# Optimization experiments

Hardware: AMD Instinct MI355X
Metric: run time of the kernel (lower is better)

Reference implementation:

```python
import jax, jax.numpy as jnp
import numpy as np

HEADS, DIM_HEADS = 16, 16
SCALE = DIM_HEADS ** -0.5

# (forward_perm, inverse_perm) for each axial dim of x: (B, S, E, H, W)
# axial axes are 1 (seq), 3 (H=4), 4 (W=5); emb axis 2 moved to last, axial axis to second-last
_PERMS = [
    ((0, 3, 4, 1, 2), (0, 3, 4, 1, 2)),  # seq axis (self-inverse)
    ((0, 1, 4, 3, 2), (0, 1, 4, 3, 2)),  # H axis (self-inverse)
    ((0, 1, 3, 4, 2), (0, 1, 4, 2, 3)),  # W axis
]


def _self_attn(x, wq, wkv, wo_w, wo_b):
    # x: (..., t, d); standard multi-head self-attention along t
    q = x @ wq.T                               # (..., t, 256)
    k, v = jnp.split(x @ wkv.T, 2, axis=-1)    # each (..., t, 256)
    lead, tlen = x.shape[:-2], x.shape[-2]
    sh = (*lead, tlen, HEADS, DIM_HEADS)
    q, k, v = q.reshape(sh), k.reshape(sh), v.reshape(sh)
    scores = jnp.einsum('...thd,...shd->...hts', q, k) * SCALE
    attn = jax.nn.softmax(scores, axis=-1)
    o = jnp.einsum('...hts,...shd->...thd', attn, v)
    o = o.reshape(*lead, tlen, HEADS * DIM_HEADS)
    return o @ wo_w.T + wo_b


def _axial_attention_layer(x, wq_l, wkv_l, wo_w_l, wo_b_l):
    # sum of attention along each axial dim (sum_axial_out=True)
    out = jnp.zeros_like(x)
    for a, (p, ip) in enumerate(_PERMS):
        y = jnp.transpose(x, p)
        y = _self_attn(y, wq_l[a], wkv_l[a], wo_w_l[a], wo_b_l[a])
        out = out + jnp.transpose(y, ip)
    return out


def setup_inputs() -> dict:
    key = jax.random.key(0)
    ks = jax.random.split(key, 8)
    B, S, E, H, W = 32, 64, 256, 4, 5
    return {
        'x': jax.random.normal(ks[0], (B, S, E, H, W), jnp.float32),
        'pos_s': jax.random.normal(ks[1], (1, S, E, 1, 1), jnp.float32),
        'pos_h': jax.random.normal(ks[2], (1, 1, E, H, 1), jnp.float32),
        'pos_w': jax.random.normal(ks[3], (1, 1, E, 1, W), jnp.float32),
        'wq': jax.random.normal(ks[4], (2, 3, 256, E), jnp.float32) * 0.02,
        'wkv': jax.random.normal(ks[5], (2, 3, 512, E), jnp.float32) * 0.02,
        'wo_w': jax.random.normal(ks[6], (2, 3, E, 256), jnp.float32) * 0.02,
        'wo_b': jnp.zeros((2, 3, E), jnp.float32),
        'dec_w': jax.random.normal(ks[7], (1, E), jnp.float32) * 0.02,
        'dec_b': jnp.zeros((1,), jnp.float32),
    }


def reference(x, pos_s, pos_h, pos_w, wq, wkv, wo_w, wo_b, dec_w, dec_b):
    # additive axial positional embeddings
    x = x + pos_s + pos_h + pos_w
    # two stacked AxialAttention blocks (no residual in the wrapper)
    for l in range(2):
        x = _axial_attention_layer(x, wq[l], wkv[l], wo_w[l], wo_b[l])
    # (B, S, E, H, W) -> (B, S, H, W, E), linear decode to 1 channel, sigmoid
    x = jnp.transpose(x, (0, 1, 3, 4, 2))
    return jax.nn.sigmoid(x @ dec_w.T + dec_b)
```

## Files before the change

kernel.cpp:

```cpp
#include <hip/hip_runtime.h>
#include <stdint.h>

typedef unsigned short u16;
typedef u16 u16x8 __attribute__((ext_vector_type(8)));
typedef __bf16 bf16x8 __attribute__((ext_vector_type(8)));
typedef float f32x4 __attribute__((ext_vector_type(4)));
typedef float f32x16 __attribute__((ext_vector_type(16)));

#define NE   256
#define NPOS 40960

__device__ __forceinline__ float bf2f(u16 h) {
  union { unsigned u; float f; } c; c.u = ((unsigned)h) << 16; return c.f;
}
__device__ __forceinline__ u16 f2bf(float f) {
  union { float f; unsigned u; } c; c.f = f;
  unsigned u = c.u;
  return (u16)((u + 0x7FFFu + ((u >> 16) & 1u)) >> 16);
}
__device__ __forceinline__ unsigned pkbf(float a, float b) {
  unsigned r;
  asm("v_cvt_pk_bf16_f32 %0, %1, %2" : "=v"(r) : "v"(a), "v"(b));
  return r;
}
__device__ __forceinline__ void gll16(const void* g, void* l) {
  __builtin_amdgcn_global_load_lds(
      (const __attribute__((address_space(1))) void*)g,
      (__attribute__((address_space(3))) void*)l, 16, 0, 0);
}

__global__ __launch_bounds__(256) void prep_kernel(
    const float* __restrict__ x, const float* __restrict__ pos_s,
    const float* __restrict__ pos_h, const float* __restrict__ pos_w,
    u16* __restrict__ xb)
{
  __shared__ float Ls[256 * 21];
  const int bs = blockIdx.x;
  const int s  = bs & 63;
  const int tid = threadIdx.x;
  const float* xp = x + (size_t)bs * 5120;
  for (int i = tid; i < 5120; i += 256) {
    int e = i / 20, hw = i % 20;
    int h = hw / 5, w = hw % 5;
    float v = xp[i] + pos_s[s * 256 + e] + pos_h[e * 4 + h] + pos_w[e * 5 + w];
    Ls[e * 21 + hw] = v;
  }
  __syncthreads();
  u16* op = xb + (size_t)bs * 20 * 256;
  for (int i = tid; i < 5120; i += 256) {
    int nl = i >> 8, e = i & 255;
    op[nl * 256 + e] = f2bf(Ls[e * 21 + nl]);
  }
}

__global__ __launch_bounds__(256) void pack_qkv(
    const float* __restrict__ wq, const float* __restrict__ wkv, u16* __restrict__ dst)
{
  int i = blockIdx.x * 256 + threadIdx.x;
  int la = i / (768 * 256);
  int rem = i - la * (768 * 256);
  int r = rem >> 8, c = rem & 255;
  float v = (r < 256) ? wq[(size_t)la * 65536 + r * 256 + c]
                      : wkv[(size_t)la * 131072 + (r - 256) * 256 + c];
  dst[i] = f2bf(v);
}

__global__ __launch_bounds__(256) void pack_wo(
    const float* __restrict__ wo, u16* __restrict__ dst)
{
  int i = blockIdx.x * 256 + threadIdx.x;
  int l = i / 196608;
  int rem = i - l * 196608;
  int out = rem / 768, k = rem % 768;
  int a = k >> 8, in = k & 255;
  dst[i] = f2bf(wo[(size_t)(((l * 3 + a) * 256) + out) * 256 + in]);
}

__global__ __launch_bounds__(256) void pack_bias(
    const float* __restrict__ wo_b, float* __restrict__ bsum)
{
  int i = blockIdx.x * 256 + threadIdx.x;
  if (i < 512) {
    int l = i >> 8, c = i & 255;
    bsum[i] = wo_b[(l * 3 + 0) * 256 + c] + wo_b[(l * 3 + 1) * 256 + c]
            + wo_b[(l * 3 + 2) * 256 + c];
  }
}

template<int MODE>
__global__ __launch_bounds__(256, 2) void gemm_bt(
    const u16* __restrict__ A, const u16* __restrict__ B,
    u16* __restrict__ Cb, float* __restrict__ Cf,
    const float* __restrict__ bias, int K, int ldc)
{
  __shared__ alignas(16) u16 As[128 * 32];
  __shared__ alignas(16) u16 Bs[128 * 32];
  const int tid  = threadIdx.x;
  const int bm   = blockIdx.x, bn = blockIdx.y;
  const int lane = tid & 63, w = tid >> 6;
  const int wr   = (w >> 1) * 64, wc = (w & 1) * 64;
  const int r16  = lane & 15, khi = lane >> 4;

  f32x4 acc[4][4] = {};

  const u16* gA = A + (size_t)bm * 128 * K;
  const u16* gB = B + (size_t)bn * 128 * K;

  const int nkt = K >> 5;
  for (int kt = 0; kt < nkt; ++kt) {
    const u16* tA = gA + kt * 32;
    const u16* tB = gB + kt * 32;
    for (int i = tid; i < 512; i += 256) {
      int row = i >> 2, seg = (i & 3) << 3;
      gll16(tA + (size_t)row * K + seg, (char*)As + i * 16);
      gll16(tB + (size_t)row * K + seg, (char*)Bs + i * 16);
    }
    asm volatile("s_waitcnt vmcnt(0)" ::: "memory");
    __syncthreads();

    bf16x8 af[4], bfr[4];
    #pragma unroll
    for (int m = 0; m < 4; ++m)
      af[m] = *(const bf16x8*)(As + (wr + m * 16 + r16) * 32 + khi * 8);
    #pragma unroll
    for (int n = 0; n < 4; ++n)
      bfr[n] = *(const bf16x8*)(Bs + (wc + n * 16 + r16) * 32 + khi * 8);
    #pragma unroll
    for (int m = 0; m < 4; ++m)
      #pragma unroll
      for (int n = 0; n < 4; ++n)
        acc[m][n] = __builtin_amdgcn_mfma_f32_16x16x32_bf16(af[m], bfr[n], acc[m][n], 0, 0, 0);
    __syncthreads();
  }

  const int row0 = bm * 128 + wr + khi * 4;
  const int col0 = bn * 128 + wc + r16;
  #pragma unroll
  for (int m = 0; m < 4; ++m) {
    #pragma unroll
    for (int n = 0; n < 4; ++n) {
      int c = col0 + n * 16;
      float bv = (MODE != 0) ? bias[c] : 0.f;
      #pragma unroll
      for (int j = 0; j < 4; ++j) {
        int r = row0 + m * 16 + j;
        if (MODE == 0)      Cb[(size_t)r * ldc + c] = f2bf(acc[m][n][j]);
        else if (MODE == 1) Cf[(size_t)r * ldc + c] = acc[m][n][j] + bv;
        else                Cb[(size_t)r * ldc + c] = f2bf(acc[m][n][j] + bv);
      }
    }
  }
}

__global__ __launch_bounds__(256) void attn_seq_mfma(
    const u16* __restrict__ QKV, u16* __restrict__ Ob)
{
  const int w = threadIdx.x >> 6, lane = threadIdx.x & 63;
  const int wid = blockIdx.x * 4 + w;
  const int hd = wid & 15, g = wid >> 4;
  const int gb = g / 20, gr = g % 20;
  const int nbase = gb * 1280 + gr;
  const int lo = lane & 31, hi = lane >> 5;

  bf16x8 kf[2], qf[2];
  #pragma unroll
  for (int t = 0; t < 2; ++t) {
    size_t r = (size_t)(nbase + (lo + 32 * t) * 20) * 768;
    kf[t] = *(const bf16x8*)(QKV + r + 256 + hd * 16 + hi * 8);
    qf[t] = *(const bf16x8*)(QKV + r +       hd * 16 + hi * 8);
  }
  union { u16 a[8]; bf16x8 v; } vt[4];
  #pragma unroll
  for (int c = 0; c < 4; ++c)
    #pragma unroll
    for (int j = 0; j < 8; ++j)
      vt[c].a[j] = QKV[(size_t)(nbase + (c * 16 + hi * 8 + j) * 20) * 768
                       + 512 + hd * 16 + lo];

  f32x16 s00 = {}, s10 = {}, s01 = {}, s11 = {};
  s00 = __builtin_amdgcn_mfma_f32_32x32x16_bf16(kf[0], qf[0], s00, 0, 0, 0);
  s10 = __builtin_amdgcn_mfma_f32_32x32x16_bf16(kf[1], qf[0], s10, 0, 0, 0);
  s01 = __builtin_amdgcn_mfma_f32_32x32x16_bf16(kf[0], qf[1], s01, 0, 0, 0);
  s11 = __builtin_amdgcn_mfma_f32_32x32x16_bf16(kf[1], qf[1], s11, 0, 0, 0);

  auto run_qt = [&](f32x16 t0, f32x16 t1, int qt) {
    float m = -1e30f;
    #pragma unroll
    for (int r = 0; r < 16; ++r) { m = fmaxf(m, t0[r]); m = fmaxf(m, t1[r]); }
    m = fmaxf(m, __shfl_xor(m, 32));
    const float C = 0.36067376022f;
    float mc = m * C;
    float sum = 0.f;
    #pragma unroll
    for (int r = 0; r < 16; ++r) {
      float p0 = __builtin_amdgcn_exp2f(t0[r] * C - mc);
      float p1 = __builtin_amdgcn_exp2f(t1[r] * C - mc);
      t0[r] = p0; t1[r] = p1; sum += p0; sum += p1;
    }
    sum += __shfl_xor(sum, 32);
    float inv = __builtin_amdgcn_rcpf(sum);
    #pragma unroll
    for (int r = 0; r < 16; ++r) { t0[r] *= inv; t1[r] *= inv; }

    f32x16 oa = {};
    #pragma unroll
    for (int c = 0; c < 4; ++c) {
      const int rb = 8 * (c & 1);
      const f32x16& tt = (c < 2) ? t0 : t1;
      unsigned X0 = pkbf(tt[rb + 0], tt[rb + 1]);
      unsigned X1 = pkbf(tt[rb + 2], tt[rb + 3]);
      unsigned Y0 = pkbf(tt[rb + 4], tt[rb + 5]);
      unsigned Y1 = pkbf(tt[rb + 6], tt[rb + 7]);
      unsigned X0p = __shfl_xor((int)X0, 32), X1p = __shfl_xor((int)X1, 32);
      unsigned Y0p = __shfl_xor((int)Y0, 32), Y1p = __shfl_xor((int)Y1, 32);
      union { unsigned u[4]; bf16x8 v; } pf;
      pf.u[0] = hi ? Y0p : X0;
      pf.u[1] = hi ? Y1p : X1;
      pf.u[2] = hi ? Y0  : X0p;
      pf.u[3] = hi ? Y1  : X1p;
      oa = __builtin_amdgcn_mfma_f32_32x32x16_bf16(vt[c].v, pf.v, oa, 0, 0, 0);
    }
    unsigned P0 = pkbf(oa[0], oa[1]);
    unsigned P1 = pkbf(oa[2], oa[3]);
    unsigned P2 = pkbf(oa[4], oa[5]);
    unsigned P3 = pkbf(oa[6], oa[7]);
    unsigned sP0 = __shfl_xor((int)P0, 32), sP1 = __shfl_xor((int)P1, 32);
    unsigned sP2 = __shfl_xor((int)P2, 32), sP3 = __shfl_xor((int)P3, 32);
    union { unsigned u[4]; u16x8 v; } ov;
    ov.u[0] = hi ? sP2 : P0;
    ov.u[1] = hi ? sP3 : P1;
    ov.u[2] = hi ? P2  : sP0;
    ov.u[3] = hi ? P3  : sP1;
    u16* po = Ob + (size_t)(nbase + (qt * 32 + lo) * 20) * 768 + hd * 16 + hi * 8;
    *(u16x8*)po = ov.v;
  };
  run_qt(s00, s10, 0);
  run_qt(s01, s11, 1);
}

template<int AXIS, int T>
__global__ __launch_bounds__(256) void attn_small(
    const u16* __restrict__ QKV, u16* __restrict__ O)
{
  const int tg = blockIdx.x * 256 + threadIdx.x;
  const int hd = tg & 15, n = tg >> 4;
  int base, stp;
  if (AXIS == 1) { int h = (n % 20) / 5; base = n - h * 5; stp = 5; }
  else           { int w5 = n % 5;       base = n - w5;    stp = 1; }

  const u16* qp = QKV + (size_t)n * 768 + hd * 16;
  u16x8 q0 = *(const u16x8*)(qp), q1 = *(const u16x8*)(qp + 8);
  float q[16];
  #pragma unroll
  for (int d = 0; d < 8; ++d) { q[d] = bf2f(q0[d]) * 0.25f; q[d + 8] = bf2f(q1[d]) * 0.25f; }

  float s[T];
  float m = -1e30f;
  #pragma unroll
  for (int j = 0; j < T; ++j) {
    const u16* kp = QKV + (size_t)(base + j * stp) * 768 + 256 + hd * 16;
    u16x8 k0 = *(const u16x8*)(kp), k1 = *(const u16x8*)(kp + 8);
    float a = 0.f;
    #pragma unroll
    for (int d = 0; d < 8; ++d) a += q[d] * bf2f(k0[d]) + q[d + 8] * bf2f(k1[d]);
    s[j] = a;
    m = fmaxf(m, a);
  }
  float sum = 0.f;
  float o[16];
  #pragma unroll
  for (int d = 0; d < 16; ++d) o[d] = 0.f;
  #pragma unroll
  for (int j = 0; j < T; ++j) {
    float pj = __expf(s[j] - m);
    sum += pj;
    const u16* vp = QKV + (size_t)(base + j * stp) * 768 + 512 + hd * 16;
    u16x8 w0 = *(const u16x8*)(vp), w1 = *(const u16x8*)(vp + 8);
    #pragma unroll
    for (int d = 0; d < 8; ++d) { o[d] += pj * bf2f(w0[d]); o[d + 8] += pj * bf2f(w1[d]); }
  }
  float inv = 1.0f / sum;
  u16x8 r0, r1;
  #pragma unroll
  for (int d = 0; d < 8; ++d) { r0[d] = f2bf(o[d] * inv); r1[d] = f2bf(o[d + 8] * inv); }
  u16* po = O + (size_t)n * 768 + hd * 16;
  *(u16x8*)(po)     = r0;
  *(u16x8*)(po + 8) = r1;
}

__global__ __launch_bounds__(256) void decode_kernel(
    const float* __restrict__ xt, const float* __restrict__ dec_w,
    const float* __restrict__ dec_b, float* __restrict__ out)
{
  int wid  = threadIdx.x >> 6;
  int lane = threadIdx.x & 63;
  int n = blockIdx.x * 4 + wid;
  float4 a = *(const float4*)(xt + (size_t)n * NE + lane * 4);
  float4 b = *(const float4*)(dec_w + lane * 4);
  float acc = a.x * b.x + a.y * b.y + a.z * b.z + a.w * b.w;
  #pragma unroll
  for (int m = 1; m < 64; m <<= 1) acc += __shfl_xor(acc, m);
  if (lane == 0) out[n] = 1.0f / (1.0f + __expf(-(acc + dec_b[0])));
}

extern "C" void kernel_launch(void* const* d_in, const int* in_sizes, int n_in,
                              void* d_out, int out_size, void* d_ws, size_t ws_size,
                              hipStream_t stream) {
  const float* x     = (const float*)d_in[0];
  const float* pos_s = (const float*)d_in[1];
  const float* pos_h = (const float*)d_in[2];
  const float* pos_w = (const float*)d_in[3];
  const float* wq    = (const float*)d_in[4];
  const float* wkv   = (const float*)d_in[5];
  const float* wo_w  = (const float*)d_in[6];
  const float* wo_b  = (const float*)d_in[7];
  const float* dec_w = (const float*)d_in[8];
  const float* dec_b = (const float*)d_in[9];
  float* out = (float*)d_out;

  char* ws = (char*)d_ws;
  u16*   xb   = (u16*)ws;
  u16*   Ob   = (u16*)(ws + 20971520);
  u16*   QKV  = (u16*)(ws + 83886080);
  u16*   wqp  = (u16*)(ws + 146800768);
  u16*   wop  = (u16*)(ws + 149160064);
  float* bsum = (float*)(ws + 149946496);
  float* acc  = (float*)(ws + 83886080);

  prep_kernel<<<2048, 256, 0, stream>>>(x, pos_s, pos_h, pos_w, xb);
  pack_qkv<<<4608, 256, 0, stream>>>(wq, wkv, wqp);
  pack_wo<<<1536, 256, 0, stream>>>(wo_w, wop);
  pack_bias<<<2, 256, 0, stream>>>(wo_b, bsum);

  for (int l = 0; l < 2; ++l) {
    for (int a = 0; a < 3; ++a) {
      int la = l * 3 + a;
      gemm_bt<0><<<dim3(320, 6), 256, 0, stream>>>(
          xb, wqp + (size_t)la * 196608, QKV, nullptr, nullptr, 256, 768);
      if (a == 0)      attn_seq_mfma<<<2560, 256, 0, stream>>>(QKV, Ob);
      else if (a == 1) attn_small<1, 4><<<2560, 256, 0, stream>>>(QKV, Ob + 256);
      else             attn_small<2, 5><<<2560, 256, 0, stream>>>(QKV, Ob + 512);
    }
    if (l == 0)
      gemm_bt<3><<<dim3(320, 2), 256, 0, stream>>>(
          Ob, wop, xb, nullptr, bsum, 768, 256);
    else
      gemm_bt<1><<<dim3(320, 2), 256, 0, stream>>>(
          Ob, wop + 196608, nullptr, acc, bsum + 256, 768, 256);
  }

  decode_kernel<<<NPOS / 4, 256, 0, stream>>>(acc, dec_w, dec_b, out);
}
```

Measured before the change: 385.4 us.

## Batch H/W axis QKV projections, fuse decode into output GEMM epilogue

Merges the H- and W-axis QKV projections into one wider GEMM (1536-wide QKV row) and one combined attention kernel, cutting launches and reducing small-grid tail effects. Folds the 1/sqrt(d) query scale into the packed wq weights. Replaces the final fp32 output write plus separate decode pass with a per-tile dot against dec_w and atomic adds into a logit buffer, followed by a tiny sigmoid kernel. This removes the fp32 activation round-trip, but adds atomics and a memset and doubles the QKV workspace.

```diff
diff --git a/kernel.cpp b/kernel.cpp
--- a/kernel.cpp
+++ b/kernel.cpp
@@ -9,6 +9,7 @@
 
 #define NE   256
 #define NPOS 40960
+#define QLD  1536
 
 __device__ __forceinline__ float bf2f(u16 h) {
   union { unsigned u; float f; } c; c.u = ((unsigned)h) << 16; return c.f;
@@ -60,7 +61,7 @@
   int la = i / (768 * 256);
   int rem = i - la * (768 * 256);
   int r = rem >> 8, c = rem & 255;
-  float v = (r < 256) ? wq[(size_t)la * 65536 + r * 256 + c]
+  float v = (r < 256) ? wq[(size_t)la * 65536 + r * 256 + c] * 0.25f
                       : wkv[(size_t)la * 131072 + (r - 256) * 256 + c];
   dst[i] = f2bf(v);
 }
@@ -90,8 +91,9 @@
 template<int MODE>
 __global__ __launch_bounds__(256, 2) void gemm_bt(
     const u16* __restrict__ A, const u16* __restrict__ B,
-    u16* __restrict__ Cb, float* __restrict__ Cf,
-    const float* __restrict__ bias, int K, int ldc)
+    u16* __restrict__ Cb, const float* __restrict__ bias,
+    const float* __restrict__ dw, float* __restrict__ logit,
+    int K, int ldc)
 {
   __shared__ alignas(16) u16 As[128 * 32];
   __shared__ alignas(16) u16 Bs[128 * 32];
@@ -135,18 +137,41 @@
 
   const int row0 = bm * 128 + wr + khi * 4;
   const int col0 = bn * 128 + wc + r16;
-  #pragma unroll
-  for (int m = 0; m < 4; ++m) {
+
+  if constexpr (MODE == 4) {
+    float dwv[4], bvv[4];
     #pragma unroll
     for (int n = 0; n < 4; ++n) {
       int c = col0 + n * 16;
-      float bv = (MODE != 0) ? bias[c] : 0.f;
+      dwv[n] = dw[c];
+      bvv[n] = bias[c];
+    }
+    #pragma unroll
+    for (int m = 0; m < 4; ++m) {
       #pragma unroll
       for (int j = 0; j < 4; ++j) {
-        int r = row0 + m * 16 + j;
-        if (MODE == 0)      Cb[(size_t)r * ldc + c] = f2bf(acc[m][n][j]);
-        else if (MODE == 1) Cf[(size_t)r * ldc + c] = acc[m][n][j] + bv;
-        else                Cb[(size_t)r * ldc + c] = f2bf(acc[m][n][j] + bv);
+        float p = 0.f;
+        #pragma unroll
+        for (int n = 0; n < 4; ++n) p += (acc[m][n][j] + bvv[n]) * dwv[n];
+        p += __shfl_xor(p, 1);
+        p += __shfl_xor(p, 2);
+        p += __shfl_xor(p, 4);
+        p += __shfl_xor(p, 8);
+        if (r16 == 0) atomicAdd(&logit[row0 + m * 16 + j], p);
+      }
+    }
+  } else {
+    #pragma unroll
+    for (int m = 0; m < 4; ++m) {
+      #pragma unroll
+      for (int n = 0; n < 4; ++n) {
+        int c = col0 + n * 16;
+        float bv = (MODE == 3) ? bias[c] : 0.f;
+        #pragma unroll
+        for (int j = 0; j < 4; ++j) {
+          int r = row0 + m * 16 + j;
+          Cb[(size_t)r * ldc + c] = f2bf(acc[m][n][j] + bv);
+        }
       }
     }
   }
@@ -165,7 +190,7 @@
   bf16x8 kf[2], qf[2];
   #pragma unroll
   for (int t = 0; t < 2; ++t) {
-    size_t r = (size_t)(nbase + (lo + 32 * t) * 20) * 768;
+    size_t r = (size_t)(nbase + (lo + 32 * t) * 20) * QLD;
     kf[t] = *(const bf16x8*)(QKV + r + 256 + hd * 16 + hi * 8);
     qf[t] = *(const bf16x8*)(QKV + r +       hd * 16 + hi * 8);
   }
@@ -174,7 +199,7 @@
   for (int c = 0; c < 4; ++c)
     #pragma unroll
     for (int j = 0; j < 8; ++j)
-      vt[c].a[j] = QKV[(size_t)(nbase + (c * 16 + hi * 8 + j) * 20) * 768
+      vt[c].a[j] = QKV[(size_t)(nbase + (c * 16 + hi * 8 + j) * 20) * QLD
                        + 512 + hd * 16 + lo];
 
   f32x16 s00 = {}, s10 = {}, s01 = {}, s11 = {};
@@ -188,7 +213,7 @@
     #pragma unroll
     for (int r = 0; r < 16; ++r) { m = fmaxf(m, t0[r]); m = fmaxf(m, t1[r]); }
     m = fmaxf(m, __shfl_xor(m, 32));
-    const float C = 0.36067376022f;
+    const float C = 1.4426950408889634f;
     float mc = m * C;
     float sum = 0.f;
     #pragma unroll
@@ -238,27 +263,22 @@
   run_qt(s01, s11, 1);
 }
 
-template<int AXIS, int T>
-__global__ __launch_bounds__(256) void attn_small(
-    const u16* __restrict__ QKV, u16* __restrict__ O)
-{
-  const int tg = blockIdx.x * 256 + threadIdx.x;
-  const int hd = tg & 15, n = tg >> 4;
-  int base, stp;
-  if (AXIS == 1) { int h = (n % 20) / 5; base = n - h * 5; stp = 5; }
-  else           { int w5 = n % 5;       base = n - w5;    stp = 1; }
-
-  const u16* qp = QKV + (size_t)n * 768 + hd * 16;
+template<int T>
+__device__ __forceinline__ void attn1(
+    const u16* __restrict__ QKV, int n, int base, int stp, int hd,
+    u16* __restrict__ po)
+{
+  const u16* qp = QKV + (size_t)n * QLD + hd * 16;
   u16x8 q0 = *(const u16x8*)(qp), q1 = *(const u16x8*)(qp + 8);
   float q[16];
   #pragma unroll
-  for (int d = 0; d < 8; ++d) { q[d] = bf2f(q0[d]) * 0.25f; q[d + 8] = bf2f(q1[d]) * 0.25f; }
+  for (int d = 0; d < 8; ++d) { q[d] = bf2f(q0[d]); q[d + 8] = bf2f(q1[d]); }
 
   float s[T];
   float m = -1e30f;
   #pragma unroll
   for (int j = 0; j < T; ++j) {
-    const u16* kp = QKV + (size_t)(base + j * stp) * 768 + 256 + hd * 16;
+    const u16* kp = QKV + (size_t)(base + j * stp) * QLD + 256 + hd * 16;
     u16x8 k0 = *(const u16x8*)(kp), k1 = *(const u16x8*)(kp + 8);
     float a = 0.f;
     #pragma unroll
@@ -274,7 +294,7 @@
   for (int j = 0; j < T; ++j) {
     float pj = __expf(s[j] - m);
     sum += pj;
-    const u16* vp = QKV + (size_t)(base + j * stp) * 768 + 512 + hd * 16;
+    const u16* vp = QKV + (size_t)(base + j * stp) * QLD + 512 + hd * 16;
     u16x8 w0 = *(const u16x8*)(vp), w1 = *(const u16x8*)(vp + 8);
     #pragma unroll
     for (int d = 0; d < 8; ++d) { o[d] += pj * bf2f(w0[d]); o[d + 8] += pj * bf2f(w1[d]); }
@@ -283,24 +303,27 @@
   u16x8 r0, r1;
   #pragma unroll
   for (int d = 0; d < 8; ++d) { r0[d] = f2bf(o[d] * inv); r1[d] = f2bf(o[d + 8] * inv); }
-  u16* po = O + (size_t)n * 768 + hd * 16;
   *(u16x8*)(po)     = r0;
   *(u16x8*)(po + 8) = r1;
 }
 
-__global__ __launch_bounds__(256) void decode_kernel(
-    const float* __restrict__ xt, const float* __restrict__ dec_w,
-    const float* __restrict__ dec_b, float* __restrict__ out)
-{
-  int wid  = threadIdx.x >> 6;
-  int lane = threadIdx.x & 63;
-  int n = blockIdx.x * 4 + wid;
-  float4 a = *(const float4*)(xt + (size_t)n * NE + lane * 4);
-  float4 b = *(const float4*)(dec_w + lane * 4);
-  float acc = a.x * b.x + a.y * b.y + a.z * b.z + a.w * b.w;
-  #pragma unroll
-  for (int m = 1; m < 64; m <<= 1) acc += __shfl_xor(acc, m);
-  if (lane == 0) out[n] = 1.0f / (1.0f + __expf(-(acc + dec_b[0])));
+__global__ __launch_bounds__(256) void attn_hw(
+    const u16* __restrict__ QKV, u16* __restrict__ Ob)
+{
+  const int tg = blockIdx.x * 256 + threadIdx.x;
+  const int hd = tg & 15, n = tg >> 4;
+  int h  = (n % 20) / 5;
+  int w5 = n % 5;
+  attn1<4>(QKV,       n, n - h * 5, 5, hd, Ob + (size_t)n * 768 + 256 + hd * 16);
+  attn1<5>(QKV + 768, n, n - w5,    1, hd, Ob + (size_t)n * 768 + 512 + hd * 16);
+}
+
+__global__ __launch_bounds__(256) void sigmoid_kernel(
+    const float* __restrict__ logit, const float* __restrict__ dec_b,
+    float* __restrict__ out)
+{
+  int i = blockIdx.x * 256 + threadIdx.x;
+  out[i] = 1.0f / (1.0f + __expf(-(logit[i] + dec_b[0])));
 }
 
 extern "C" void kernel_launch(void* const* d_in, const int* in_sizes, int n_in,
@@ -319,35 +342,34 @@
   float* out = (float*)d_out;
 
   char* ws = (char*)d_ws;
-  u16*   xb   = (u16*)ws;
-  u16*   Ob   = (u16*)(ws + 20971520);
-  u16*   QKV  = (u16*)(ws + 83886080);
-  u16*   wqp  = (u16*)(ws + 146800768);
-  u16*   wop  = (u16*)(ws + 149160064);
-  float* bsum = (float*)(ws + 149946496);
-  float* acc  = (float*)(ws + 83886080);
+  u16*   xb    = (u16*)ws;
+  u16*   Ob    = (u16*)(ws + 20971520);
+  u16*   QKV   = (u16*)(ws + 83886080);
+  u16*   wqp   = (u16*)(ws + 209715200);
+  u16*   wop   = (u16*)(ws + 212074496);
+  float* bsum  = (float*)(ws + 212860928);
+  float* logit = (float*)(ws + 212862976);
 
   prep_kernel<<<2048, 256, 0, stream>>>(x, pos_s, pos_h, pos_w, xb);
   pack_qkv<<<4608, 256, 0, stream>>>(wq, wkv, wqp);
   pack_wo<<<1536, 256, 0, stream>>>(wo_w, wop);
   pack_bias<<<2, 256, 0, stream>>>(wo_b, bsum);
+  hipMemsetAsync(logit, 0, NPOS * sizeof(float), stream);
 
   for (int l = 0; l < 2; ++l) {
-    for (int a = 0; a < 3; ++a) {
-      int la = l * 3 + a;
-      gemm_bt<0><<<dim3(320, 6), 256, 0, stream>>>(
-          xb, wqp + (size_t)la * 196608, QKV, nullptr, nullptr, 256, 768);
-      if (a == 0)      attn_seq_mfma<<<2560, 256, 0, stream>>>(QKV, Ob);
-      else if (a == 1) attn_small<1, 4><<<2560, 256, 0, stream>>>(QKV, Ob + 256);
-      else             attn_small<2, 5><<<2560, 256, 0, stream>>>(QKV, Ob + 512);
-    }
+    gemm_bt<0><<<dim3(320, 6), 256, 0, stream>>>(
+        xb, wqp + (size_t)(l * 3) * 196608, QKV, nullptr, nullptr, nullptr, 256, QLD);
+    attn_seq_mfma<<<2560, 256, 0, stream>>>(QKV, Ob);
+    gemm_bt<0><<<dim3(320, 12), 256, 0, stream>>>(
+        xb, wqp + (size_t)(l * 3 + 1) * 196608, QKV, nullptr, nullptr, nullptr, 256, QLD);
+    attn_hw<<<2560, 256, 0, stream>>>(QKV, Ob);
     if (l == 0)
       gemm_bt<3><<<dim3(320, 2), 256, 0, stream>>>(
-          Ob, wop, xb, nullptr, bsum, 768, 256);
+          Ob, wop, xb, bsum, nullptr, nullptr, 768, 256);
     else
-      gemm_bt<1><<<dim3(320, 2), 256, 0, stream>>>(
-          Ob, wop + 196608, nullptr, acc, bsum + 256, 768, 256);
-  }
-
-  decode_kernel<<<NPOS / 4, 256, 0, stream>>>(acc, dec_w, dec_b, out);
-}
+      gemm_bt<4><<<dim3(320, 2), 256, 0, stream>>>(
+          Ob, wop + 196608, nullptr, bsum + 256, dec_w, logit, 768, 0);
+  }
+
+  sigmoid_kernel<<<NPOS / 256, 256, 0, stream>>>(logit, dec_b, out);
+}
```

New measurement: 367.2 us. 4.7% less time.
